# Performance work log

Measured on AMD Instinct MI355X. Metric: run time of the kernel, lower is better.

Reference implementation:

```python
import jax, jax.numpy as jnp
import numpy as np

B, T, C, H = 2, 2048, 1024, 16
D = C // H
HID = 4 * C
EPS = 1e-5


def _rmsnorm(x, w):
    return w * (x * jax.lax.rsqrt(jnp.mean(x * x, axis=-1, keepdims=True) + EPS))


def setup_inputs() -> dict:
    key = jax.random.key(0)
    ks = jax.random.split(key, 12)
    s = 0.02
    inp = {
        "x": jax.random.normal(ks[0], (B, T, C), jnp.float32),
        "mask": jnp.tril(jnp.ones((T, T), jnp.int32))[None, None],  # (1,1,T,T) causal
        "attn_norm_w": jnp.ones((C,), jnp.float32),
        "mlp_norm_w": jnp.ones((C,), jnp.float32),
        "q_w": jax.random.normal(ks[1], (C, C), jnp.float32) * s,
        "q_b": jnp.zeros((C,), jnp.float32),
        "k_w": jax.random.normal(ks[2], (C, C), jnp.float32) * s,
        "k_b": jnp.zeros((C,), jnp.float32),
        "v_w": jax.random.normal(ks[3], (C, C), jnp.float32) * s,
        "v_b": jnp.zeros((C,), jnp.float32),
        "o_w": jax.random.normal(ks[4], (C, C), jnp.float32) * s,
        "o_b": jnp.zeros((C,), jnp.float32),
        "w1": jax.random.normal(ks[5], (C, HID), jnp.float32) * s,
        "b1": jnp.zeros((HID,), jnp.float32),
        "w2": jax.random.normal(ks[6], (HID, C), jnp.float32) * s,
        "b2": jnp.zeros((C,), jnp.float32),
    }
    return inp


def reference(x, mask, attn_norm_w, mlp_norm_w, q_w, q_b, k_w, k_b, v_w, v_b,
              o_w, o_b, w1, b1, w2, b2):
    # Pre-norm path (use_post_norm=False)
    h = _rmsnorm(x, attn_norm_w)
    q = (h @ q_w + q_b).reshape(B, T, H, D).transpose(0, 2, 1, 3)  # (B,H,T,D)
    k = (h @ k_w + k_b).reshape(B, T, H, D).transpose(0, 2, 1, 3)
    v = (h @ v_w + v_b).reshape(B, T, H, D).transpose(0, 2, 1, 3)
    scores = jnp.einsum("bhqd,bhkd->bhqk", q, k) / jnp.sqrt(jnp.float32(D))
    scores = jnp.where(mask == 0, jnp.float32(-jnp.inf), scores)
    attn = jax.nn.softmax(scores, axis=-1)  # (B,H,T,T)
    ctx = jnp.einsum("bhqk,bhkd->bhqd", attn, v)
    attn_out = ctx.transpose(0, 2, 1, 3).reshape(B, T, C) @ o_w + o_b
    x = x + attn_out
    m = _rmsnorm(x, mlp_norm_w)
    mlp_out = jax.nn.gelu(m @ w1 + b1, approximate=False) @ w2 + b2
    x = x + mlp_out
    return (x, k, v)
```

## Files before the change

kernel.cpp:

```cpp
#include <hip/hip_runtime.h>
#include <hip/hip_bf16.h>


#define B_ 2
#define T_ 2048
#define C_ 1024
#define H_ 16
#define D_ 64
#define HID_ 4096
#define M_ 4096
#define NQKV 3072

typedef __bf16 bf16x8 __attribute__((ext_vector_type(8)));
typedef float f32x4 __attribute__((ext_vector_type(4)));
using bf16 = __hip_bfloat16;

#define WAIT_VM(N) asm volatile("s_waitcnt vmcnt(" #N ")" ::: "memory")
#define SBAR() asm volatile("s_barrier" ::: "memory")

static __device__ __forceinline__ f32x4 mfma16(bf16x8 a, bf16x8 b, f32x4 c) {
  return __builtin_amdgcn_mfma_f32_16x16x32_bf16(a, b, c, 0, 0, 0);
}

static __device__ __forceinline__ void gload16(const bf16* g, bf16* l) {
  __builtin_amdgcn_global_load_lds(
      (const __attribute__((address_space(1))) unsigned int*)g,
      (__attribute__((address_space(3))) unsigned int*)l, 16, 0, 0);
}

static __device__ __forceinline__ unsigned short bfbits(float x) {
  __hip_bfloat16 h = __float2bfloat16(x);
  return *(unsigned short*)&h;
}

static __device__ __forceinline__ float gelu_tanh(float v) {
  float z = 0.7978845608f * (v + 0.044715f * v * v * v);
  float az = fabsf(z);
  float e = __expf(-2.0f * az);
  float th = (1.0f - e) / (1.0f + e);
  th = copysignf(th, z);
  return 0.5f * v * (1.0f + th);
}

__global__ __launch_bounds__(256) void cvt_transpose(const float* __restrict__ in,
                                                     bf16* __restrict__ out, int K, int N) {
  __shared__ float tile[32][33];
  int tid = threadIdx.x, tx = tid & 31, ty = tid >> 5;
  int n0 = blockIdx.x * 32, k0 = blockIdx.y * 32;
#pragma unroll
  for (int i = 0; i < 4; ++i) {
    int r = ty + i * 8;
    tile[r][tx] = in[(size_t)(k0 + r) * N + n0 + tx];
  }
  __syncthreads();
#pragma unroll
  for (int i = 0; i < 4; ++i) {
    int r = ty + i * 8;
    out[(size_t)(n0 + r) * K + k0 + tx] = __float2bfloat16(tile[tx][r]);
  }
}

__global__ __launch_bounds__(256) void pack_bias(const float* __restrict__ q,
                                                 const float* __restrict__ k,
                                                 const float* __restrict__ v,
                                                 float* __restrict__ o) {
  int i = blockIdx.x * 256 + threadIdx.x;
  o[i] = i < 1024 ? q[i] : (i < 2048 ? k[i - 1024] : v[i - 2048]);
}

__global__ __launch_bounds__(256) void rmsnorm_kernel(const float* __restrict__ x,
                                                      const float* __restrict__ w,
                                                      bf16* __restrict__ out) {
  int row = blockIdx.x, tid = threadIdx.x;
  float4 v = ((const float4*)(x + (size_t)row * C_))[tid];
  float ss = v.x * v.x + v.y * v.y + v.z * v.z + v.w * v.w;
#pragma unroll
  for (int d = 1; d < 64; d <<= 1) ss += __shfl_xor(ss, d);
  __shared__ float wsum[4];
  if ((tid & 63) == 0) wsum[tid >> 6] = ss;
  __syncthreads();
  float tot = wsum[0] + wsum[1] + wsum[2] + wsum[3];
  float r = rsqrtf(tot * (1.0f / C_) + 1e-5f);
  float4 wv = ((const float4*)w)[tid];
  bf16* o = out + (size_t)row * C_ + tid * 4;
  o[0] = __float2bfloat16(v.x * wv.x * r);
  o[1] = __float2bfloat16(v.y * wv.y * r);
  o[2] = __float2bfloat16(v.z * wv.z * r);
  o[3] = __float2bfloat16(v.w * wv.w * r);
}

__global__ __launch_bounds__(256) void qkv_post(const bf16* __restrict__ Cq,
                                                bf16* __restrict__ vtb,
                                                float* __restrict__ kout,
                                                float* __restrict__ vout) {
  __shared__ unsigned short vt[64][33];
  int tid = threadIdx.x, bh = blockIdx.y, t0 = blockIdx.x * 32;
  int b = bh >> 4, hh = bh & 15;
  int row = tid >> 3, db8 = (tid & 7) * 8;
  const bf16* Ck = Cq + (size_t)(b * 2048 + t0) * NQKV + 1024 + hh * 64;
  bf16x8 kv = *(const bf16x8*)&Ck[(size_t)row * NQKV + db8];
  float* kd = kout + ((size_t)bh * 2048 + t0 + row) * 64 + db8;
#pragma unroll
  for (int j = 0; j < 8; ++j) kd[j] = (float)kv[j];
  bf16x8 vv = *(const bf16x8*)&Ck[(size_t)row * NQKV + 1024 + db8];
  const unsigned short* vb = (const unsigned short*)&vv;
  float* vd = vout + ((size_t)bh * 2048 + t0 + row) * 64 + db8;
#pragma unroll
  for (int j = 0; j < 8; ++j) {
    vd[j] = (float)vv[j];
    vt[db8 + j][row] = vb[j];
  }
  __syncthreads();
  int d = tid >> 2, t8 = (tid & 3) * 8;
  union { unsigned short u[8]; bf16x8 v8; } o;
#pragma unroll
  for (int j = 0; j < 8; ++j) o.u[j] = vt[d][t8 + j];
  *(bf16x8*)&vtb[((size_t)bh * 64 + d) * 2048 + t0 + t8] = o.v8;
}

template <int EPI, int DBUF, int SK>
__global__ __launch_bounds__(256) void gemm_kernel(
    const bf16* __restrict__ A, const bf16* __restrict__ Bt, const float* __restrict__ bias,
    bf16* __restrict__ bfout, float* __restrict__ fout, const float* __restrict__ res,
    float* __restrict__ paux, const float* __restrict__ bias2, int M, int N, int K) {
  __shared__ bf16 Al[(DBUF ? 2 : 1) * 128 * 64];
  __shared__ bf16 Bl[(DBUF ? 2 : 1) * 128 * 64];
  int tid = threadIdx.x, w = tid >> 6, l = tid & 63;
  int g = l >> 4, c = l & 15;
  int nwg = gridDim.x * gridDim.y;
  int bidl = blockIdx.y * gridDim.x + blockIdx.x;
  int wgid = (bidl & 7) * (nwg >> 3) + (bidl >> 3);
  int bx = wgid % gridDim.x, by = wgid / gridDim.x;
  int m0 = by * 128, n0 = bx * 128;
  int wm = (w >> 1) * 64, wn = (w & 1) * 64;
  int Kc = K / SK;
  int kbase = (SK > 1) ? (int)blockIdx.z * Kc : 0;
  int KT = Kc >> 6;
  int lrow = l >> 3;
  int sgr = (l & 7) ^ lrow;

  const bf16* gA = A + (size_t)(m0 + w * 32 + lrow) * K + kbase + sgr * 8;
  const bf16* gB = Bt + (size_t)(n0 + w * 32 + lrow) * K + kbase + sgr * 8;

  auto stage = [&](int kt, int buf) {
#pragma unroll
    for (int i = 0; i < 4; ++i) {
      gload16(gA + (size_t)i * 8 * K + kt * 64, Al + buf * 8192 + (w * 4 + i) * 512);
      gload16(gB + (size_t)i * 8 * K + kt * 64, Bl + buf * 8192 + (w * 4 + i) * 512);
    }
  };
  auto compute = [&](int buf, f32x4 (&acc)[4][4]) {
#pragma unroll
    for (int ch = 0; ch < 2; ++ch) {
      bf16x8 af[4], bfr[4];
#pragma unroll
      for (int f = 0; f < 4; ++f)
        af[f] = *(const bf16x8*)&Al[buf * 8192 + (wm + f * 16 + c) * 64 +
                                    (((ch * 4 + g) ^ (c & 7)) << 3)];
#pragma unroll
      for (int f = 0; f < 4; ++f)
        bfr[f] = *(const bf16x8*)&Bl[buf * 8192 + (wn + f * 16 + c) * 64 +
                                     (((ch * 4 + g) ^ (c & 7)) << 3)];
#pragma unroll
      for (int mf = 0; mf < 4; ++mf)
#pragma unroll
        for (int nf = 0; nf < 4; ++nf) acc[mf][nf] = mfma16(af[mf], bfr[nf], acc[mf][nf]);
    }
  };

  f32x4 acc[4][4] = {};
  if (DBUF) {
    stage(0, 0);
    for (int kt = 0; kt < KT; ++kt) {
      int cur = kt & 1;
      if (kt + 1 < KT) {
        stage(kt + 1, cur ^ 1);
        WAIT_VM(8);
      } else {
        WAIT_VM(0);
      }
      SBAR();
      __builtin_amdgcn_s_setprio(1);
      compute(cur, acc);
      __builtin_amdgcn_s_setprio(0);
      __builtin_amdgcn_sched_barrier(0);
      SBAR();
    }
  } else {
    for (int kt = 0; kt < KT; ++kt) {
      stage(kt, 0);
      __syncthreads();
      compute(0, acc);
      __syncthreads();
    }
  }

#pragma unroll
  for (int mf = 0; mf < 4; ++mf) {
#pragma unroll
    for (int nf = 0; nf < 4; ++nf) {
      int gn = n0 + wn + nf * 16 + c;
      float bv = bias ? bias[gn] : 0.f;
#pragma unroll
      for (int r = 0; r < 4; ++r) {
        int gm = m0 + wm + mf * 16 + g * 4 + r;
        float vr = acc[mf][nf][r];
        float v = vr + bv;
        if (EPI == 4) {
          atomicAdd(fout + (size_t)gm * N + gn, vr);
        } else if (SK > 1 && blockIdx.z > 0) {
          paux[(size_t)gm * N + gn] = vr;
        } else if (EPI == 5) {
          bfout[(size_t)gm * N + gn] = __float2bfloat16(v);
        } else if (EPI == 3) {
          size_t idx = (size_t)gm * N + gn;
          float t = v + res[idx];
          fout[idx] = t;
          paux[idx] = t + bias2[gn];
        } else {
          size_t idx = (size_t)gm * N + gn;
          bfout[idx] = __float2bfloat16(gelu_tanh(v));
        }
      }
    }
  }
}

__global__ __launch_bounds__(256, 2) void attn_kernel(const bf16* __restrict__ Cq,
                                                      const bf16* __restrict__ Vt,
                                                      bf16* __restrict__ o0p,
                                                      bf16* __restrict__ o1p,
                                                      float* __restrict__ ml) {
  constexpr int LDP = 72;
  __shared__ bf16 Kl[2][64 * 64];
  __shared__ bf16 Vl[2][64 * 64];
  __shared__ bf16 Pl[4][2][16 * LDP];
  __shared__ float alw[4][2][16];
  int tid = threadIdx.x, w = tid >> 6, l = tid & 63, g = l >> 4, c = l & 15;
  int bid = blockIdx.x;
  int bh = bid & 31;
  int rest = bid >> 5;
  int qt = 15 - (rest >> 1);
  int half = rest & 1;
  int qbase = qt * 128 + w * 32;
  int b = bh >> 4, hh = bh & 15;
  const bf16* Qh = Cq + (size_t)(b * 2048) * NQKV + hh * 64;
  const bf16* Kh = Qh + 1024;
  const bf16* Vh = Vt + (size_t)bh * T_ * D_;

  int NT = 2 * qt + 2, H0 = qt + 1;
  int t0 = half ? H0 : 0, t1 = half ? NT : H0;

  int srow = l >> 3;
  int sce = ((l & 7) * 8) ^ (srow << 3);
  int cswz = (c & 7) << 3;

  auto stage = [&](int ti, int buf) {
#pragma unroll
    for (int i = 0; i < 2; ++i) {
      int row = i * 32 + w * 8 + srow;
      gload16(&Kh[(size_t)(ti * 64 + row) * NQKV + sce], &Kl[buf][i * 2048 + w * 512]);
      gload16(&Vh[(size_t)row * T_ + ti * 64 + sce], &Vl[buf][i * 2048 + w * 512]);
    }
  };

  stage(t0, 0);

  bf16x8 aq[2][2];
#pragma unroll
  for (int qf = 0; qf < 2; ++qf)
#pragma unroll
    for (int ch = 0; ch < 2; ++ch)
      aq[qf][ch] =
          *(const bf16x8*)&Qh[(size_t)(qbase + qf * 16 + c) * NQKV + ch * 32 + g * 8];

  f32x4 o[2][4] = {};
  float mrun[2] = {-1e30f, -1e30f};
  float lrun[2] = {0.f, 0.f};

  __syncthreads();

  for (int ti = t0; ti < t1; ++ti) {
    int cur = (ti - t0) & 1;
    int kv0 = ti * 64;
    if (ti + 1 < t1) stage(ti + 1, cur ^ 1);

    f32x4 sf[2][4];
#pragma unroll
    for (int kb = 0; kb < 4; ++kb) {
      bf16x8 bk0 = *(const bf16x8*)&Kl[cur][(kb * 16 + c) * 64 + ((g * 8) ^ cswz)];
      bf16x8 bk1 = *(const bf16x8*)&Kl[cur][(kb * 16 + c) * 64 + ((32 + g * 8) ^ cswz)];
#pragma unroll
      for (int qf = 0; qf < 2; ++qf) {
        f32x4 t = {};
        t = mfma16(bk0, aq[qf][0], t);
        t = mfma16(bk1, aq[qf][1], t);
        sf[qf][kb] = t;
      }
    }

    float s[2][4][4];
#pragma unroll
    for (int qf = 0; qf < 2; ++qf)
#pragma unroll
      for (int kb = 0; kb < 4; ++kb)
#pragma unroll
        for (int r = 0; r < 4; ++r) s[qf][kb][r] = sf[qf][kb][r] * 0.125f;
    if (kv0 + 63 > qbase) {
#pragma unroll
      for (int qf = 0; qf < 2; ++qf)
#pragma unroll
        for (int kb = 0; kb < 4; ++kb)
#pragma unroll
          for (int r = 0; r < 4; ++r) {
            int qi = qbase + qf * 16 + c;
            int kv = kv0 + kb * 16 + g * 4 + r;
            if (kv > qi) s[qf][kb][r] = -3.0e38f;
          }
    }

#pragma unroll
    for (int qf = 0; qf < 2; ++qf) {
      float m01 = fmaxf(fmaxf(s[qf][0][0], s[qf][0][1]), fmaxf(s[qf][0][2], s[qf][0][3]));
      float m23 = fmaxf(fmaxf(s[qf][1][0], s[qf][1][1]), fmaxf(s[qf][1][2], s[qf][1][3]));
      float m45 = fmaxf(fmaxf(s[qf][2][0], s[qf][2][1]), fmaxf(s[qf][2][2], s[qf][2][3]));
      float m67 = fmaxf(fmaxf(s[qf][3][0], s[qf][3][1]), fmaxf(s[qf][3][2], s[qf][3][3]));
      float tm = fmaxf(fmaxf(m01, m23), fmaxf(m45, m67));
      tm = fmaxf(tm, __shfl_xor(tm, 16));
      tm = fmaxf(tm, __shfl_xor(tm, 32));
      float mn = fmaxf(mrun[qf], tm);
      float al = __expf(mrun[qf] - mn);
      mrun[qf] = mn;
      float asum = 0.f;
#pragma unroll
      for (int kb = 0; kb < 4; ++kb)
#pragma unroll
        for (int r = 0; r < 4; ++r) {
          float pv = __expf(s[qf][kb][r] - mn);
          s[qf][kb][r] = pv;
          asum += pv;
        }
      asum += __shfl_xor(asum, 16);
      asum += __shfl_xor(asum, 32);
      lrun[qf] = lrun[qf] * al + asum;
      if (l < 16) alw[w][qf][c] = al;
    }

#pragma unroll
    for (int qf = 0; qf < 2; ++qf)
#pragma unroll
      for (int kb = 0; kb < 4; ++kb) {
        union { unsigned short u[4]; uint2 v2; } pk;
#pragma unroll
        for (int r = 0; r < 4; ++r) pk.u[r] = bfbits(s[qf][kb][r]);
        *(uint2*)&Pl[w][qf][c * LDP + kb * 16 + g * 4] = pk.v2;
      }

#pragma unroll
    for (int qf = 0; qf < 2; ++qf) {
      f32x4 a4 = *(const f32x4*)&alw[w][qf][g * 4];
#pragma unroll
      for (int db = 0; db < 4; ++db)
#pragma unroll
        for (int r = 0; r < 4; ++r) o[qf][db][r] *= a4[r];
    }

    bf16x8 bvv[4][2];
#pragma unroll
    for (int db = 0; db < 4; ++db)
#pragma unroll
      for (int ck = 0; ck < 2; ++ck)
        bvv[db][ck] = *(const bf16x8*)&Vl[cur][(db * 16 + c) * 64 + ((ck * 32 + g * 8) ^ cswz)];

#pragma unroll
    for (int qf = 0; qf < 2; ++qf) {
      bf16x8 pa0 = *(const bf16x8*)&Pl[w][qf][c * LDP + g * 8];
      bf16x8 pa1 = *(const bf16x8*)&Pl[w][qf][c * LDP + 32 + g * 8];
#pragma unroll
      for (int db = 0; db < 4; ++db) {
        o[qf][db] = mfma16(pa0, bvv[db][0], o[qf][db]);
        o[qf][db] = mfma16(pa1, bvv[db][1], o[qf][db]);
      }
    }
    __syncthreads();
  }

  bf16* op = half ? o1p : o0p;
  int rowbase = bh * 2048 + qt * 128 + w * 32;
#pragma unroll
  for (int qf = 0; qf < 2; ++qf)
#pragma unroll
    for (int r = 0; r < 4; ++r)
#pragma unroll
      for (int db = 0; db < 4; ++db)
        op[(size_t)(rowbase + qf * 16 + g * 4 + r) * 64 + db * 16 + c] =
            __float2bfloat16(o[qf][db][r]);
  if (l < 16) {
    float* mh = ml + half * 131072;
#pragma unroll
    for (int qf = 0; qf < 2; ++qf) {
      mh[rowbase + qf * 16 + c] = mrun[qf];
      mh[65536 + rowbase + qf * 16 + c] = lrun[qf];
    }
  }
}

__global__ __launch_bounds__(256) void merge_attn(const bf16* __restrict__ o0,
                                                  const bf16* __restrict__ o1,
                                                  const float* __restrict__ ml,
                                                  bf16* __restrict__ ctx) {
  int idx = blockIdx.x * 256 + threadIdx.x;
  int row = idx >> 2, dc = (idx & 3) * 16;
  float m0 = ml[row], l0 = ml[65536 + row];
  float m1 = ml[131072 + row], l1 = ml[196608 + row];
  float Mx = fmaxf(m0, m1);
  float s0 = __expf(m0 - Mx), s1 = __expf(m1 - Mx);
  float inv = 1.0f / (l0 * s0 + l1 * s1);
  const bf16x8* p0 = (const bf16x8*)&o0[(size_t)row * 64 + dc];
  const bf16x8* p1 = (const bf16x8*)&o1[(size_t)row * 64 + dc];
  bf16x8 a0 = p0[0], a1 = p0[1], b0 = p1[0], b1 = p1[1];
  int bh = row >> 11, t = row & 2047;
  int b_ = bh >> 4, hh = bh & 15;
  bf16* dst = ctx + ((size_t)(b_ * T_ + t)) * C_ + hh * D_ + dc;
#pragma unroll
  for (int j = 0; j < 8; ++j) {
    dst[j] = __float2bfloat16(((float)a0[j] * s0 + (float)b0[j] * s1) * inv);
    dst[8 + j] = __float2bfloat16(((float)a1[j] * s0 + (float)b1[j] * s1) * inv);
  }
}

extern "C" void kernel_launch(void* const* d_in, const int* in_sizes, int n_in, void* d_out,
                              int out_size, void* d_ws, size_t ws_size, hipStream_t stream) {
  const float* x = (const float*)d_in[0];
  const float* anw = (const float*)d_in[2];
  const float* mnw = (const float*)d_in[3];
  const float* q_w = (const float*)d_in[4];
  const float* q_b = (const float*)d_in[5];
  const float* k_w = (const float*)d_in[6];
  const float* k_b = (const float*)d_in[7];
  const float* v_w = (const float*)d_in[8];
  const float* v_b = (const float*)d_in[9];
  const float* o_w = (const float*)d_in[10];
  const float* o_b = (const float*)d_in[11];
  const float* w1 = (const float*)d_in[12];
  const float* b1 = (const float*)d_in[13];
  const float* w2 = (const float*)d_in[14];
  const float* b2 = (const float*)d_in[15];
  float* out = (float*)d_out;
  char* ws = (char*)d_ws;

  bf16* owT = (bf16*)(ws + 0);
  bf16* w1T = (bf16*)(ws + 2097152);
  bf16* w2T = (bf16*)(ws + 10485760);
  bf16* h = (bf16*)(ws + 18874368);
  bf16* qkvT = (bf16*)(ws + 27262976);
  bf16* Cq = (bf16*)(ws + 33554432);
  bf16* vtb = (bf16*)(ws + 58720256);
  bf16* o0p = (bf16*)(ws + 67108864);
  bf16* o1p = (bf16*)(ws + 75497472);
  float* ml = (float*)(ws + 27262976);
  float* qkvb = (float*)(ws + 67108864);
  bf16* ctx = (bf16*)(ws + 33554432);
  float* x2 = (float*)(ws + 41943040);
  bf16* m = h;
  bf16* hid = (bf16*)(ws + 50331648);

  cvt_transpose<<<dim3(32, 32), 256, 0, stream>>>(q_w, qkvT, 1024, 1024);
  cvt_transpose<<<dim3(32, 32), 256, 0, stream>>>(k_w, qkvT + 1048576, 1024, 1024);
  cvt_transpose<<<dim3(32, 32), 256, 0, stream>>>(v_w, qkvT + 2097152, 1024, 1024);
  cvt_transpose<<<dim3(32, 32), 256, 0, stream>>>(o_w, owT, 1024, 1024);
  cvt_transpose<<<dim3(128, 32), 256, 0, stream>>>(w1, w1T, 1024, 4096);
  cvt_transpose<<<dim3(32, 128), 256, 0, stream>>>(w2, w2T, 4096, 1024);
  pack_bias<<<12, 256, 0, stream>>>(q_b, k_b, v_b, qkvb);

  rmsnorm_kernel<<<4096, 256, 0, stream>>>(x, anw, h);

  gemm_kernel<5, 0, 1><<<dim3(24, 32), 256, 0, stream>>>(
      h, qkvT, qkvb, Cq, nullptr, nullptr, nullptr, nullptr, 4096, 3072, 1024);

  qkv_post<<<dim3(64, 32), 256, 0, stream>>>(Cq, vtb, out + 4194304, out + 8388608);

  attn_kernel<<<1024, 256, 0, stream>>>(Cq, vtb, o0p, o1p, ml);
  merge_attn<<<1024, 256, 0, stream>>>(o0p, o1p, ml, ctx);

  gemm_kernel<3, 1, 1><<<dim3(8, 32), 256, 0, stream>>>(
      ctx, owT, o_b, nullptr, x2, x, out, b2, 4096, 1024, 1024);

  rmsnorm_kernel<<<4096, 256, 0, stream>>>(x2, mnw, m);

  gemm_kernel<2, 0, 1><<<dim3(32, 32), 256, 0, stream>>>(
      m, w1T, b1, hid, nullptr, nullptr, nullptr, nullptr, 4096, 4096, 1024);
  gemm_kernel<4, 1, 2><<<dim3(8, 32, 2), 256, 0, stream>>>(
      hid, w2T, nullptr, nullptr, out, nullptr, nullptr, nullptr, 4096, 1024, 4096);
}
```

Measured before the change: 277.5 us.

## Add 8-wave 256x128 triple-buffered GEMM for QKV, MLP up and down projections

Adds a new GEMM kernel using 512 threads (8 waves) with 256x128 tiles and a three-stage LDS ring. Global-to-LDS loads for tile t+2 are interleaved with the MFMA work on tile t, split into two half-phases per k-step with barriers and priority hints. The QKV, MLP-up and split-K MLP-down GEMMs now use it, while the old kernel is kept only for the output-projection epilogue. The larger tiles and deeper pipeline aim to hide memory latency and improve operand reuse, at the cost of more LDS per block (roughly 144 KB), more barriers, and fewer blocks per GEMM.

```diff
diff --git a/kernel.cpp b/kernel.cpp
--- a/kernel.cpp
+++ b/kernel.cpp
@@ -16,6 +16,7 @@
 using bf16 = __hip_bfloat16;
 
 #define WAIT_VM(N) asm volatile("s_waitcnt vmcnt(" #N ")" ::: "memory")
+#define WAIT_LGKM0() asm volatile("s_waitcnt lgkmcnt(0)" ::: "memory")
 #define SBAR() asm volatile("s_barrier" ::: "memory")
 
 static __device__ __forceinline__ f32x4 mfma16(bf16x8 a, bf16x8 b, f32x4 c) {
@@ -118,13 +119,120 @@
   *(bf16x8*)&vtb[((size_t)bh * 64 + d) * 2048 + t0 + t8] = o.v8;
 }
 
-template <int EPI, int DBUF, int SK>
+template <int EPI, int SK>
+__global__ __launch_bounds__(512, 2) void gemm8p(
+    const bf16* __restrict__ A, const bf16* __restrict__ Bt, const float* __restrict__ bias,
+    bf16* __restrict__ bfout, float* __restrict__ fout, int M, int N, int K) {
+  __shared__ bf16 As[3][256 * 64];
+  __shared__ bf16 Bs[3][128 * 64];
+  int tid = threadIdx.x, wid = tid >> 6, l = tid & 63, g = l >> 4, c = l & 15;
+  int wm = wid >> 2, wn = wid & 3;
+  int nwg = gridDim.x * gridDim.y;
+  int bidl = blockIdx.y * gridDim.x + blockIdx.x;
+  int wgid = (bidl & 7) * (nwg >> 3) + (bidl >> 3);
+  int bx = wgid % gridDim.x, by = wgid / gridDim.x;
+  int m0 = by * 256, n0 = bx * 128;
+  int Kc = K / SK;
+  int kbase = (SK > 1) ? (int)blockIdx.z * Kc : 0;
+  int NT = Kc >> 6;
+
+  int srow = tid >> 3;
+  int scol = ((tid & 7) ^ (srow & 7)) << 3;
+  const bf16* gA = A + (size_t)(m0 + srow) * K + kbase + scol;
+  const bf16* gB = Bt + (size_t)(n0 + srow) * K + kbase + scol;
+
+  auto stA = [&](int t, int j) {
+    gload16(gA + (size_t)j * 64 * K + t * 64, &As[t % 3][wid * 512 + j * 4096]);
+  };
+  auto stB = [&](int t, int j) {
+    gload16(gB + (size_t)j * 64 * K + t * 64, &Bs[t % 3][wid * 512 + j * 4096]);
+  };
+
+  f32x4 acc[8][2] = {};
+#pragma unroll
+  for (int j = 0; j < 4; ++j) stA(0, j);
+  stB(0, 0); stB(0, 1);
+#pragma unroll
+  for (int j = 0; j < 4; ++j) stA(1, j);
+  stB(1, 0); stB(1, 1);
+
+  for (int t = 0; t < NT; ++t) {
+    if (t == NT - 1) { WAIT_VM(0); } else { WAIT_VM(6); }
+    SBAR();
+    int s = t % 3;
+    bf16x8 bfr[2][2];
+#pragma unroll
+    for (int q = 0; q < 2; ++q) {
+      bf16x8 af[4][2];
+      if (q == 0) {
+#pragma unroll
+        for (int nf = 0; nf < 2; ++nf)
+#pragma unroll
+          for (int kk = 0; kk < 2; ++kk) {
+            int row = wn * 32 + nf * 16 + c;
+            bfr[nf][kk] =
+                *(const bf16x8*)&Bs[s][row * 64 + (((kk * 4 + g) ^ (row & 7)) << 3)];
+          }
+      }
+#pragma unroll
+      for (int i = 0; i < 4; ++i)
+#pragma unroll
+        for (int kk = 0; kk < 2; ++kk) {
+          int row = wm * 128 + (q * 4 + i) * 16 + c;
+          af[i][kk] =
+              *(const bf16x8*)&As[s][row * 64 + (((kk * 4 + g) ^ (row & 7)) << 3)];
+        }
+      if (t + 2 < NT) {
+        if (q == 0) { stA(t + 2, 0); stA(t + 2, 1); stA(t + 2, 2); }
+        else        { stA(t + 2, 3); stB(t + 2, 0); stB(t + 2, 1); }
+      }
+      SBAR();
+      WAIT_LGKM0();
+      __builtin_amdgcn_sched_barrier(0);
+      __builtin_amdgcn_s_setprio(1);
+#pragma unroll
+      for (int i = 0; i < 4; ++i)
+#pragma unroll
+        for (int nf = 0; nf < 2; ++nf)
+#pragma unroll
+          for (int kk = 0; kk < 2; ++kk)
+            acc[q * 4 + i][nf] = mfma16(af[i][kk], bfr[nf][kk], acc[q * 4 + i][nf]);
+      __builtin_amdgcn_s_setprio(0);
+      __builtin_amdgcn_sched_barrier(0);
+      SBAR();
+    }
+  }
+
+#pragma unroll
+  for (int mf = 0; mf < 8; ++mf) {
+#pragma unroll
+    for (int nf = 0; nf < 2; ++nf) {
+      int gn = n0 + wn * 32 + nf * 16 + c;
+      float bv = bias ? bias[gn] : 0.f;
+#pragma unroll
+      for (int r = 0; r < 4; ++r) {
+        int gm = m0 + wm * 128 + mf * 16 + g * 4 + r;
+        float vr = acc[mf][nf][r];
+        float v = vr + bv;
+        if (EPI == 4) {
+          atomicAdd(fout + (size_t)gm * N + gn, vr);
+        } else if (EPI == 5) {
+          bfout[(size_t)gm * N + gn] = __float2bfloat16(v);
+        } else {
+          bfout[(size_t)gm * N + gn] = __float2bfloat16(gelu_tanh(v));
+        }
+      }
+    }
+  }
+}
+
+template <int EPI>
 __global__ __launch_bounds__(256) void gemm_kernel(
     const bf16* __restrict__ A, const bf16* __restrict__ Bt, const float* __restrict__ bias,
-    bf16* __restrict__ bfout, float* __restrict__ fout, const float* __restrict__ res,
-    float* __restrict__ paux, const float* __restrict__ bias2, int M, int N, int K) {
-  __shared__ bf16 Al[(DBUF ? 2 : 1) * 128 * 64];
-  __shared__ bf16 Bl[(DBUF ? 2 : 1) * 128 * 64];
+    float* __restrict__ fout, const float* __restrict__ res, float* __restrict__ paux,
+    const float* __restrict__ bias2, int M, int N, int K) {
+  __shared__ bf16 Al[2 * 128 * 64];
+  __shared__ bf16 Bl[2 * 128 * 64];
   int tid = threadIdx.x, w = tid >> 6, l = tid & 63;
   int g = l >> 4, c = l & 15;
   int nwg = gridDim.x * gridDim.y;
@@ -133,14 +241,12 @@
   int bx = wgid % gridDim.x, by = wgid / gridDim.x;
   int m0 = by * 128, n0 = bx * 128;
   int wm = (w >> 1) * 64, wn = (w & 1) * 64;
-  int Kc = K / SK;
-  int kbase = (SK > 1) ? (int)blockIdx.z * Kc : 0;
-  int KT = Kc >> 6;
+  int KT = K >> 6;
   int lrow = l >> 3;
   int sgr = (l & 7) ^ lrow;
 
-  const bf16* gA = A + (size_t)(m0 + w * 32 + lrow) * K + kbase + sgr * 8;
-  const bf16* gB = Bt + (size_t)(n0 + w * 32 + lrow) * K + kbase + sgr * 8;
+  const bf16* gA = A + (size_t)(m0 + w * 32 + lrow) * K + sgr * 8;
+  const bf16* gB = Bt + (size_t)(n0 + w * 32 + lrow) * K + sgr * 8;
 
   auto stage = [&](int kt, int buf) {
 #pragma unroll
@@ -169,30 +275,21 @@
   };
 
   f32x4 acc[4][4] = {};
-  if (DBUF) {
-    stage(0, 0);
-    for (int kt = 0; kt < KT; ++kt) {
-      int cur = kt & 1;
-      if (kt + 1 < KT) {
-        stage(kt + 1, cur ^ 1);
-        WAIT_VM(8);
-      } else {
-        WAIT_VM(0);
-      }
-      SBAR();
-      __builtin_amdgcn_s_setprio(1);
-      compute(cur, acc);
-      __builtin_amdgcn_s_setprio(0);
-      __builtin_amdgcn_sched_barrier(0);
-      SBAR();
-    }
-  } else {
-    for (int kt = 0; kt < KT; ++kt) {
-      stage(kt, 0);
-      __syncthreads();
-      compute(0, acc);
-      __syncthreads();
-    }
+  stage(0, 0);
+  for (int kt = 0; kt < KT; ++kt) {
+    int cur = kt & 1;
+    if (kt + 1 < KT) {
+      stage(kt + 1, cur ^ 1);
+      WAIT_VM(8);
+    } else {
+      WAIT_VM(0);
+    }
+    SBAR();
+    __builtin_amdgcn_s_setprio(1);
+    compute(cur, acc);
+    __builtin_amdgcn_s_setprio(0);
+    __builtin_amdgcn_sched_barrier(0);
+    SBAR();
   }
 
 #pragma unroll
@@ -200,27 +297,15 @@
 #pragma unroll
     for (int nf = 0; nf < 4; ++nf) {
       int gn = n0 + wn + nf * 16 + c;
-      float bv = bias ? bias[gn] : 0.f;
+      float bv = bias[gn];
 #pragma unroll
       for (int r = 0; r < 4; ++r) {
         int gm = m0 + wm + mf * 16 + g * 4 + r;
-        float vr = acc[mf][nf][r];
-        float v = vr + bv;
-        if (EPI == 4) {
-          atomicAdd(fout + (size_t)gm * N + gn, vr);
-        } else if (SK > 1 && blockIdx.z > 0) {
-          paux[(size_t)gm * N + gn] = vr;
-        } else if (EPI == 5) {
-          bfout[(size_t)gm * N + gn] = __float2bfloat16(v);
-        } else if (EPI == 3) {
-          size_t idx = (size_t)gm * N + gn;
-          float t = v + res[idx];
-          fout[idx] = t;
-          paux[idx] = t + bias2[gn];
-        } else {
-          size_t idx = (size_t)gm * N + gn;
-          bfout[idx] = __float2bfloat16(gelu_tanh(v));
-        }
+        float v = acc[mf][nf][r] + bv;
+        size_t idx = (size_t)gm * N + gn;
+        float t = v + res[idx];
+        fout[idx] = t;
+        paux[idx] = t + bias2[gn];
       }
     }
   }
@@ -475,21 +560,21 @@
 
   rmsnorm_kernel<<<4096, 256, 0, stream>>>(x, anw, h);
 
-  gemm_kernel<5, 0, 1><<<dim3(24, 32), 256, 0, stream>>>(
-      h, qkvT, qkvb, Cq, nullptr, nullptr, nullptr, nullptr, 4096, 3072, 1024);
+  gemm8p<5, 1><<<dim3(24, 16), 512, 0, stream>>>(h, qkvT, qkvb, Cq, nullptr,
+                                                 4096, 3072, 1024);
 
   qkv_post<<<dim3(64, 32), 256, 0, stream>>>(Cq, vtb, out + 4194304, out + 8388608);
 
   attn_kernel<<<1024, 256, 0, stream>>>(Cq, vtb, o0p, o1p, ml);
   merge_attn<<<1024, 256, 0, stream>>>(o0p, o1p, ml, ctx);
 
-  gemm_kernel<3, 1, 1><<<dim3(8, 32), 256, 0, stream>>>(
-      ctx, owT, o_b, nullptr, x2, x, out, b2, 4096, 1024, 1024);
+  gemm_kernel<3><<<dim3(8, 32), 256, 0, stream>>>(ctx, owT, o_b, x2, x, out, b2,
+                                                  4096, 1024, 1024);
 
   rmsnorm_kernel<<<4096, 256, 0, stream>>>(x2, mnw, m);
 
-  gemm_kernel<2, 0, 1><<<dim3(32, 32), 256, 0, stream>>>(
-      m, w1T, b1, hid, nullptr, nullptr, nullptr, nullptr, 4096, 4096, 1024);
-  gemm_kernel<4, 1, 2><<<dim3(8, 32, 2), 256, 0, stream>>>(
-      hid, w2T, nullptr, nullptr, out, nullptr, nullptr, nullptr, 4096, 1024, 4096);
-}
+  gemm8p<2, 1><<<dim3(32, 16), 512, 0, stream>>>(m, w1T, b1, hid, nullptr,
+                                                 4096, 4096, 1024);
+  gemm8p<4, 2><<<dim3(8, 16, 2), 512, 0, stream>>>(hid, w2T, nullptr, nullptr, out,
+                                                   4096, 1024, 4096);
+}
```

New measurement: 279.4 us. About the same (+0.7%).

## Merge weight prep launches into one kernel and double-buffer every GEMM

Applied to the files above, without the earlier changes.

Replaces six transpose-convert launches and the bias pack launch with a single prep_all kernel that picks its source matrix by block index, which removes launch overhead and tail gaps between small kernels. It also removes the single-buffer GEMM path, so the QKV and W1 GEMMs now use the double-buffered LDS pipeline with async prefetch. LDS use per block doubles for those GEMMs, which may lower occupancy.

```diff
diff --git a/kernel.cpp b/kernel.cpp
--- a/kernel.cpp
+++ b/kernel.cpp
@@ -42,30 +42,50 @@
   return 0.5f * v * (1.0f + th);
 }
 
-__global__ __launch_bounds__(256) void cvt_transpose(const float* __restrict__ in,
-                                                     bf16* __restrict__ out, int K, int N) {
-  __shared__ float tile[32][33];
-  int tid = threadIdx.x, tx = tid & 31, ty = tid >> 5;
-  int n0 = blockIdx.x * 32, k0 = blockIdx.y * 32;
+__global__ __launch_bounds__(256) void prep_all(
+    const float* __restrict__ q_w, const float* __restrict__ k_w,
+    const float* __restrict__ v_w, const float* __restrict__ o_w,
+    const float* __restrict__ w1, const float* __restrict__ w2,
+    const float* __restrict__ q_b, const float* __restrict__ k_b,
+    const float* __restrict__ v_b, bf16* __restrict__ qkvT, bf16* __restrict__ owT,
+    bf16* __restrict__ w1T, bf16* __restrict__ w2T, float* __restrict__ qkvb) {
+  int bid = blockIdx.x, tid = threadIdx.x;
+  if (bid >= 12288) {
+    int i = (bid - 12288) * 256 + tid;
+    qkvb[i] = i < 1024 ? q_b[i] : (i < 2048 ? k_b[i - 1024] : v_b[i - 2048]);
+    return;
+  }
+  const float* in;
+  bf16* out;
+  int K, N, tile;
+  if (bid < 4096) {
+    int which = bid >> 10;
+    tile = bid & 1023;
+    K = 1024; N = 1024;
+    if (which == 0) { in = q_w; out = qkvT; }
+    else if (which == 1) { in = k_w; out = qkvT + 1048576; }
+    else if (which == 2) { in = v_w; out = qkvT + 2097152; }
+    else { in = o_w; out = owT; }
+  } else if (bid < 8192) {
+    tile = bid - 4096; K = 1024; N = 4096; in = w1; out = w1T;
+  } else {
+    tile = bid - 8192; K = 4096; N = 1024; in = w2; out = w2T;
+  }
+  int ntx = N >> 5;
+  int n0 = (tile % ntx) * 32, k0 = (tile / ntx) * 32;
+  __shared__ float t32[32][33];
+  int tx = tid & 31, ty = tid >> 5;
 #pragma unroll
   for (int i = 0; i < 4; ++i) {
     int r = ty + i * 8;
-    tile[r][tx] = in[(size_t)(k0 + r) * N + n0 + tx];
+    t32[r][tx] = in[(size_t)(k0 + r) * N + n0 + tx];
   }
   __syncthreads();
 #pragma unroll
   for (int i = 0; i < 4; ++i) {
     int r = ty + i * 8;
-    out[(size_t)(n0 + r) * K + k0 + tx] = __float2bfloat16(tile[tx][r]);
-  }
-}
-
-__global__ __launch_bounds__(256) void pack_bias(const float* __restrict__ q,
-                                                 const float* __restrict__ k,
-                                                 const float* __restrict__ v,
-                                                 float* __restrict__ o) {
-  int i = blockIdx.x * 256 + threadIdx.x;
-  o[i] = i < 1024 ? q[i] : (i < 2048 ? k[i - 1024] : v[i - 2048]);
+    out[(size_t)(n0 + r) * K + k0 + tx] = __float2bfloat16(t32[tx][r]);
+  }
 }
 
 __global__ __launch_bounds__(256) void rmsnorm_kernel(const float* __restrict__ x,
@@ -118,13 +138,13 @@
   *(bf16x8*)&vtb[((size_t)bh * 64 + d) * 2048 + t0 + t8] = o.v8;
 }
 
-template <int EPI, int DBUF, int SK>
+template <int EPI, int SK>
 __global__ __launch_bounds__(256) void gemm_kernel(
     const bf16* __restrict__ A, const bf16* __restrict__ Bt, const float* __restrict__ bias,
     bf16* __restrict__ bfout, float* __restrict__ fout, const float* __restrict__ res,
     float* __restrict__ paux, const float* __restrict__ bias2, int M, int N, int K) {
-  __shared__ bf16 Al[(DBUF ? 2 : 1) * 128 * 64];
-  __shared__ bf16 Bl[(DBUF ? 2 : 1) * 128 * 64];
+  __shared__ bf16 Al[2 * 128 * 64];
+  __shared__ bf16 Bl[2 * 128 * 64];
   int tid = threadIdx.x, w = tid >> 6, l = tid & 63;
   int g = l >> 4, c = l & 15;
   int nwg = gridDim.x * gridDim.y;
@@ -169,30 +189,21 @@
   };
 
   f32x4 acc[4][4] = {};
-  if (DBUF) {
-    stage(0, 0);
-    for (int kt = 0; kt < KT; ++kt) {
-      int cur = kt & 1;
-      if (kt + 1 < KT) {
-        stage(kt + 1, cur ^ 1);
-        WAIT_VM(8);
-      } else {
-        WAIT_VM(0);
-      }
-      SBAR();
-      __builtin_amdgcn_s_setprio(1);
-      compute(cur, acc);
-      __builtin_amdgcn_s_setprio(0);
-      __builtin_amdgcn_sched_barrier(0);
-      SBAR();
-    }
-  } else {
-    for (int kt = 0; kt < KT; ++kt) {
-      stage(kt, 0);
-      __syncthreads();
-      compute(0, acc);
-      __syncthreads();
-    }
+  stage(0, 0);
+  for (int kt = 0; kt < KT; ++kt) {
+    int cur = kt & 1;
+    if (kt + 1 < KT) {
+      stage(kt + 1, cur ^ 1);
+      WAIT_VM(8);
+    } else {
+      WAIT_VM(0);
+    }
+    SBAR();
+    __builtin_amdgcn_s_setprio(1);
+    compute(cur, acc);
+    __builtin_amdgcn_s_setprio(0);
+    __builtin_amdgcn_sched_barrier(0);
+    SBAR();
   }
 
 #pragma unroll
@@ -465,17 +476,12 @@
   bf16* m = h;
   bf16* hid = (bf16*)(ws + 50331648);
 
-  cvt_transpose<<<dim3(32, 32), 256, 0, stream>>>(q_w, qkvT, 1024, 1024);
-  cvt_transpose<<<dim3(32, 32), 256, 0, stream>>>(k_w, qkvT + 1048576, 1024, 1024);
-  cvt_transpose<<<dim3(32, 32), 256, 0, stream>>>(v_w, qkvT + 2097152, 1024, 1024);
-  cvt_transpose<<<dim3(32, 32), 256, 0, stream>>>(o_w, owT, 1024, 1024);
-  cvt_transpose<<<dim3(128, 32), 256, 0, stream>>>(w1, w1T, 1024, 4096);
-  cvt_transpose<<<dim3(32, 128), 256, 0, stream>>>(w2, w2T, 4096, 1024);
-  pack_bias<<<12, 256, 0, stream>>>(q_b, k_b, v_b, qkvb);
+  prep_all<<<12300, 256, 0, stream>>>(q_w, k_w, v_w, o_w, w1, w2, q_b, k_b, v_b,
+                                      qkvT, owT, w1T, w2T, qkvb);
 
   rmsnorm_kernel<<<4096, 256, 0, stream>>>(x, anw, h);
 
-  gemm_kernel<5, 0, 1><<<dim3(24, 32), 256, 0, stream>>>(
+  gemm_kernel<5, 1><<<dim3(24, 32), 256, 0, stream>>>(
       h, qkvT, qkvb, Cq, nullptr, nullptr, nullptr, nullptr, 4096, 3072, 1024);
 
   qkv_post<<<dim3(64, 32), 256, 0, stream>>>(Cq, vtb, out + 4194304, out + 8388608);
@@ -483,13 +489,13 @@
   attn_kernel<<<1024, 256, 0, stream>>>(Cq, vtb, o0p, o1p, ml);
   merge_attn<<<1024, 256, 0, stream>>>(o0p, o1p, ml, ctx);
 
-  gemm_kernel<3, 1, 1><<<dim3(8, 32), 256, 0, stream>>>(
+  gemm_kernel<3, 1><<<dim3(8, 32), 256, 0, stream>>>(
       ctx, owT, o_b, nullptr, x2, x, out, b2, 4096, 1024, 1024);
 
   rmsnorm_kernel<<<4096, 256, 0, stream>>>(x2, mnw, m);
 
-  gemm_kernel<2, 0, 1><<<dim3(32, 32), 256, 0, stream>>>(
+  gemm_kernel<2, 1><<<dim3(32, 32), 256, 0, stream>>>(
       m, w1T, b1, hid, nullptr, nullptr, nullptr, nullptr, 4096, 4096, 1024);
-  gemm_kernel<4, 1, 2><<<dim3(8, 32, 2), 256, 0, stream>>>(
+  gemm_kernel<4, 2><<<dim3(8, 32, 2), 256, 0, stream>>>(
       hid, w2T, nullptr, nullptr, out, nullptr, nullptr, nullptr, 4096, 1024, 4096);
 }
```

Result: faster. 262.6 us (-5.3%).
